# Optimization experiments

Measured on AMD Instinct MI355X. Metric: run time of the kernel, lower is better.

Reference implementation:

```python
import jax, jax.numpy as jnp
import numpy as np

B, C_IN, C_OUT, N, T, KT = 8, 32, 64, 512, 24, 3
EPS = 1e-5

def leaky(x):
    return jax.nn.leaky_relu(x, 0.01)

def layer_norm(x, g, b):
    # LayerNorm over last 3 dims [C_OUT, N, T]
    m = x.mean(axis=(1, 2, 3), keepdims=True)
    v = x.var(axis=(1, 2, 3), keepdims=True)
    return (x - m) * jax.lax.rsqrt(v + EPS) * g[None] + b[None]

def conv1d_dil2(x, w):
    # Conv1d(kernel=2, dilation=2, padding=1, no bias); x: (B,C,L), w: (O,C,2)
    return jax.lax.conv_general_dilated(x, w, window_strides=(1,), padding=[(1, 1)],
                                        rhs_dilation=(2,), dimension_numbers=('NCH', 'OIH', 'NCH'))

def setup_inputs():
    key = jax.random.key(0)
    ks = jax.random.split(key, 32)
    x = jax.random.normal(ks[0], (B, C_IN, N, T), jnp.float32)
    mask = jax.random.uniform(ks[1], (N, N)) < 0.02
    adj = jnp.where(mask, jax.random.uniform(ks[2], (N, N)), 0.0).astype(jnp.float32)
    s = 0.05
    p = {
        'conv1_w': jax.random.normal(ks[3], (C_OUT, C_IN)) * s,
        'conv1_b': jnp.zeros((C_OUT,)),
        'tc_w': jax.random.normal(ks[4], (C_OUT, C_IN, 1, KT)) * s,
        'tc_b': jnp.zeros((C_OUT,)),
        'ln_g': jnp.ones((C_OUT, N, T)),
        'ln_b': jnp.zeros((C_OUT, N, T)),
        's0_ws': jax.random.normal(ks[5], (T, T)) * s,
        's0_wn': jax.random.normal(ks[6], (T, T)) * s,
        's0_b': jnp.zeros((T,)),
        's1_ws': jax.random.normal(ks[7], (T, T)) * s,
        's1_wn': jax.random.normal(ks[8], (T, T)) * s,
        's1_b': jnp.zeros((T,)),
        't_w1': jax.random.normal(ks[9], (C_OUT,)) * s,
        't_w2': jax.random.normal(ks[10], (N,)) * s,
        't_wd1': jax.random.normal(ks[11], (T, T, 2)) * s,
        't_wd2': jax.random.normal(ks[12], (C_OUT, C_OUT, 2)) * s,
        't_W': jax.random.normal(ks[13], (N, C_OUT)) * s,
        't_b': jnp.zeros((T, T)),
        't_v': jax.random.normal(ks[14], (T, T)) * s,
        'bn_g': jnp.ones((T,)),
        'bn_b': jnp.zeros((T,)),
    }
    return {'x': x, 'adj': adj, **p}

def _forward(x, adj, conv1_w, conv1_b, tc_w, tc_b, ln_g, ln_b,
             s0_ws, s0_wn, s0_b, s1_ws, s1_wn, s1_b,
             t_w1, t_w2, t_wd1, t_wd2, t_W, t_b, t_v, bn_g, bn_b):
    # 1x1 conv residual branch
    x_input = jnp.einsum('bcnl,oc->bonl', x, conv1_w) + conv1_b[None, :, None, None]
    # temporal conv (1,Kt) padding (0,1)
    x1 = jax.lax.conv_general_dilated(x, tc_w, (1, 1), [(0, 0), (1, 1)],
                                      dimension_numbers=('NCHW', 'OIHW', 'NCHW'))
    x1 = x1 + tc_b[None, :, None, None]
    x1 = leaky(layer_norm(x1, ln_g, ln_b))
    Ls = jnp.stack([jnp.eye(N, dtype=x.dtype) * 4.0, adj])          # (2,N,N)
    h = jnp.einsum('bcnl,knq->bckql', x1, Ls)                        # (B,C_OUT,2,N,T)
    M = (adj != 0).astype(x.dtype)                                   # edges u->v
    deg = jnp.maximum(M.sum(axis=0), 1.0)                            # in-degree per dst
    def sage(h, ws, wn, bias):
        neigh = jnp.einsum('bckul,uv->bckvl', h, M) / deg[None, None, None, :, None]
        return (jnp.einsum('bcknl,ml->bcknm', h, ws)
                + jnp.einsum('bcknl,ml->bcknm', neigh, wn) + bias)
    h = sage(h, s0_ws, s0_wn, s0_b)
    h = sage(h, s1_ws, s1_wn, s1_b)
    x1 = h.reshape(B, 2 * C_OUT, N, T)
    filt, gate = x1[:, :C_OUT], x1[:, C_OUT:]
    x1 = jax.nn.sigmoid(gate) * leaky(filt)                          # (B,C_OUT,N,T)
    # TATT_1
    f1 = jnp.einsum('bcnl,c->bln', x1, t_w1)                         # (B,T,N)
    f1 = conv1d_dil2(f1, t_wd1)                                      # (B,T,N)
    f2 = jnp.einsum('bcnl,n->bcl', x1, t_w2)                         # (B,C_OUT,T)
    f2 = conv1d_dil2(f2, t_wd2)                                      # (B,C_OUT,T)
    logits = jax.nn.sigmoid(jnp.einsum('bln,nc,bcq->blq', f1, t_W, f2) + t_b)
    logits = jnp.einsum('lk,bkq->blq', t_v, logits)                  # (B,T,T)
    # BatchNorm1d(T) on permuted (B,T_q,T_l), training-mode batch stats
    z = logits.transpose(0, 2, 1)
    mu = z.mean(axis=(0, 2), keepdims=True)
    var = z.var(axis=(0, 2), keepdims=True)
    z = (z - mu) * jax.lax.rsqrt(var + EPS) * bn_g[None, :, None] + bn_b[None, :, None]
    logits = z.transpose(0, 2, 1)
    A = np.zeros((T, T), np.float32); A[:12, :12] = 1.0; A[12:, 12:] = 1.0
    Bmask = jnp.asarray(-1e13 * (1.0 - A), jnp.float32)
    coefs = jax.nn.softmax(logits + Bmask, axis=-1)                  # (B,T,T)
    T_coef = coefs.transpose(0, 2, 1)
    x1 = jnp.einsum('bcnl,blq->bcnq', x1, T_coef)
    out = layer_norm(leaky(x1) + x_input, ln_g, ln_b)
    return out, adj, T_coef

def reference(x, adj, conv1_w, conv1_b, tc_w, tc_b, ln_g, ln_b,
              s0_ws, s0_wn, s0_b, s1_ws, s1_wn, s1_b,
              t_w1, t_w2, t_wd1, t_wd2, t_W, t_b, t_v, bn_g, bn_b):
    return _forward(x, adj, conv1_w, conv1_b, tc_w, tc_b, ln_g, ln_b,
                    s0_ws, s0_wn, s0_b, s1_ws, s1_wn, s1_b,
                    t_w1, t_w2, t_wd1, t_wd2, t_W, t_b, t_v, bn_g, bn_b)
```

## Files before the change

kernel.cpp:

```cpp
#include <hip/hip_runtime.h>
#include <hip/hip_bf16.h>
#include <math.h>

#define B_    8
#define CIN   32
#define CO    64
#define NN    512
#define TT    24
#define NT    (NN*TT)
#define LNCNT (CO*NT)
#define EPSL  1e-5f
#define MAXNZ 64
#define HSS   28

typedef const float* fp;
static __device__ __forceinline__ float lk(float x){ return x > 0.f ? x : 0.01f*x; }
static __device__ __forceinline__ float sg(float x){
    if(x >= 0.f){ float e = expf(-x); return 1.f/(1.f+e); }
    float e = expf(x); return e/(1.f+e);
}
static __device__ __forceinline__ unsigned pk2(float a, float b){
    __hip_bfloat16 x = __float2bfloat16(a), y = __float2bfloat16(b);
    unsigned lo = *(unsigned short*)&x, hi = *(unsigned short*)&y;
    return lo | (hi<<16);
}
static __device__ __forceinline__ float lo2f(unsigned u){ return __uint_as_float(u<<16); }
static __device__ __forceinline__ float hi2f(unsigned u){ return __uint_as_float(u & 0xffff0000u); }

__global__ __launch_bounds__(256) void k_csc(fp adj, int* cnt, int* idx, float* val,
        float* o_adj){
    int e = blockIdx.x*blockDim.x + threadIdx.x;
    if(e >= NN*NN) return;
    float a = adj[e];
    o_adj[e] = a;
    if(a != 0.f){
        int u = e >> 9, q = e & 511;
        int slot = atomicAdd(&cnt[q], 1);
        if(slot < MAXNZ){ idx[q*MAXNZ+slot] = u; val[q*MAXNZ+slot] = a; }
    }
}

static __device__ __forceinline__ void ldw_split(fp w, int m, int kb, uint4* hi, uint4* lo){
    float vh[8], vl[8];
    #pragma unroll
    for(int j=0;j<8;++j){
        float v = (m < TT && (kb+j) < TT) ? w[m*TT + kb + j] : 0.f;
        __hip_bfloat16 hb = __float2bfloat16(v);
        float hf = __bfloat162float(hb);
        vh[j] = hf;
        vl[j] = v - hf;
    }
    *hi = make_uint4(pk2(vh[0],vh[1]),pk2(vh[2],vh[3]),pk2(vh[4],vh[5]),pk2(vh[6],vh[7]));
    *lo = make_uint4(pk2(vl[0],vl[1]),pk2(vl[2],vl[3]),pk2(vl[4],vl[5]),pk2(vl[6],vl[7]));
}

__global__ __launch_bounds__(256) void k_wprep(fp s0ws, fp s0wn, fp s1ws, fp s1wn, uint4* wf,
        fp w1, fp wt, uint4* wcf){
    int t = threadIdx.x;
    int lane = t & 63, g = t >> 6;
    {
        int M = g >> 1, H = g & 1;
        int m  = H*16 + (lane&15);
        int kb = (lane>>4)*8;
        for(int L=0; L<2; ++L){
            fp w = L ? (M ? s1wn : s1ws) : (M ? s0wn : s0ws);
            uint4 hi, lo;
            ldw_split(w, m, kb, &hi, &lo);
            wf[L*512 + g*128 +      lane] = hi;
            wf[L*512 + g*128 + 64 + lane] = lo;
        }
    }
    {
        int kb = (lane>>4)*8;
        for(int ot=0; ot<4; ++ot){
            int m = ot*16 + (lane&15);
            float vh[8], vl[8];
            #pragma unroll
            for(int j=0;j<8;++j){
                int c = kb+j;
                float v = (g==0) ? w1[m*CIN+c] : wt[(m*CIN+c)*3 + (g-1)];
                __hip_bfloat16 hb = __float2bfloat16(v);
                float hf = __bfloat162float(hb);
                vh[j]=hf; vl[j]=v-hf;
            }
            wcf[ot*512 + g*128 +      lane] = make_uint4(
                pk2(vh[0],vh[1]),pk2(vh[2],vh[3]),pk2(vh[4],vh[5]),pk2(vh[6],vh[7]));
            wcf[ot*512 + g*128 + 64 + lane] = make_uint4(
                pk2(vl[0],vl[1]),pk2(vl[2],vl[3]),pk2(vl[4],vl[5]),pk2(vl[6],vl[7]));
        }
    }
}

typedef __attribute__((ext_vector_type(8))) short bf16x8;
typedef __attribute__((ext_vector_type(4))) float f32x4;
typedef __attribute__((ext_vector_type(2))) float f32x2;

static __device__ __forceinline__ f32x4 MF(uint4 a, uint4 b, f32x4 c){
    union { uint4 u; bf16x8 v; } A, Bv; A.u = a; Bv.u = b;
    return __builtin_amdgcn_mfma_f32_16x16x32_bf16(A.v, Bv.v, c, 0, 0, 0);
}

#define XST 20
__global__ __launch_bounds__(256, 4) void k_conv(fp x, const uint4* wcf, fp b1, fp bt,
        float* xin, float* x1p, float* stats){
    __shared__ __attribute__((aligned(16))) unsigned xh[208*XST];
    __shared__ __attribute__((aligned(16))) unsigned xl[208*XST];
    __shared__ float red[256];
    int bid = blockIdx.x; int b = bid>>6; int n0 = (bid&63)*8;
    int tid = threadIdx.x; int lane = tid&63; int w = tid>>6;
    for(int i=tid;i<3072;i+=256){
        int cp = i/192; int r = i-cp*192; int node = r/24; int t = r-node*24;
        const float* xp = x + ((size_t)(b*CIN + 2*cp)*NN + n0+node)*TT + t;
        float a = xp[0], b2 = xp[NT];
        __hip_bfloat16 ab = __float2bfloat16(a), bb = __float2bfloat16(b2);
        float ah = __bfloat162float(ab), bh = __bfloat162float(bb);
        int row = node*26 + t + 1;
        xh[row*XST+cp] = pk2(ah, bh);
        xl[row*XST+cp] = pk2(a-ah, b2-bh);
    }
    {
        int node = tid>>5; int which = (tid>>4)&1; int j = tid&15;
        int row = node*26 + which*25;
        xh[row*XST+j]=0; xl[row*XST+j]=0;
    }
    const uint4* wb = wcf + w*512;
    uint4 h1 = wb[      lane], l1 = wb[ 64+lane];
    uint4 ht0= wb[128 + lane], lt0= wb[192+lane];
    uint4 ht1= wb[256 + lane], lt1= wb[320+lane];
    uint4 ht2= wb[384 + lane], lt2= wb[448+lane];
    int mrow = (lane>>4)*4;
    float bi0[4], bi1[4];
    #pragma unroll
    for(int r2=0;r2<4;++r2){
        int o = w*16 + mrow + r2;
        bi0[r2]=b1[o]; bi1[r2]=bt[o];
    }
    __syncthreads();
    float ls=0.f, lsq=0.f;
    int kb4 = (lane>>4)*4;
    for(int pt=0; pt<12; ++pt){
        int p = pt*16 + (lane&15);
        int node = p/24, t = p-node*24;
        int rc = (node*26 + t + 1)*XST;
        uint4 Bhm = *(const uint4*)&xh[rc - XST + kb4];
        uint4 Blm = *(const uint4*)&xl[rc - XST + kb4];
        uint4 Bhc = *(const uint4*)&xh[rc       + kb4];
        uint4 Blc = *(const uint4*)&xl[rc       + kb4];
        uint4 Bhp = *(const uint4*)&xh[rc + XST + kb4];
        uint4 Blp = *(const uint4*)&xl[rc + XST + kb4];
        f32x4 D0 = {bi0[0],bi0[1],bi0[2],bi0[3]};
        f32x4 D1 = {bi1[0],bi1[1],bi1[2],bi1[3]};
        D0 = MF(h1, Bhc, D0); D0 = MF(l1, Bhc, D0); D0 = MF(h1, Blc, D0);
        D1 = MF(ht0,Bhm, D1); D1 = MF(lt0,Bhm, D1); D1 = MF(ht0,Blm, D1);
        D1 = MF(ht1,Bhc, D1); D1 = MF(lt1,Bhc, D1); D1 = MF(ht1,Blc, D1);
        D1 = MF(ht2,Bhp, D1); D1 = MF(lt2,Bhp, D1); D1 = MF(ht2,Blp, D1);
        size_t gbase = ((size_t)(b*CO + w*16 + mrow)*NN + n0+node)*TT + t;
        #pragma unroll
        for(int r2=0;r2<4;++r2){
            xin[gbase + (size_t)r2*NT] = D0[r2];
            x1p[gbase + (size_t)r2*NT] = D1[r2];
            ls  += D1[r2];
            lsq += D1[r2]*D1[r2];
        }
    }
    red[tid]=ls; __syncthreads();
    for(int s=128;s>0;s>>=1){ if(tid<s) red[tid]+=red[tid+s]; __syncthreads(); }
    float tsum = red[0]; __syncthreads();
    red[tid]=lsq; __syncthreads();
    for(int s=128;s>0;s>>=1){ if(tid<s) red[tid]+=red[tid+s]; __syncthreads(); }
    if(tid==0){ atomicAdd(&stats[b], tsum); atomicAdd(&stats[8+b], red[0]); }
}

__global__ __launch_bounds__(512, 4) void k_hbuild(fp x1p, fp lng, fp lnb,
        const float* stats, const int* cnt, const int* idx, const float* val, unsigned* h){
    __shared__ float xs[NN*HSS];
    int blk = blockIdx.x; int b = blk >> 6; int c = blk & 63;
    int tid = threadIdx.x;
    float mm = stats[b] / (float)LNCNT;
    float vv = fmaxf(stats[8+b] / (float)LNCNT - mm*mm, 0.f);
    float m = mm, inv = rsqrtf(vv + EPSL);
    fp src  = x1p + (size_t)(b*CO + c)*NT;
    fp gsrc = lng + (size_t)c*NT;
    fp bsrc = lnb + (size_t)c*NT;
    for(int i4=tid;i4<NT/4;i4+=512){
        int i = i4*4;
        int n = i/TT, t = i-n*TT;
        float4 s  = *(const float4*)(src + i);
        float4 g  = *(const float4*)(gsrc + i);
        float4 bb = *(const float4*)(bsrc + i);
        *(float4*)&xs[n*HSS + t] = make_float4(
            lk((s.x-m)*inv*g.x+bb.x), lk((s.y-m)*inv*g.y+bb.y),
            lk((s.z-m)*inv*g.z+bb.z), lk((s.w-m)*inv*g.w+bb.w));
    }
    int n = tid;
    int c0 = cnt[n];
    int cq = c0 > MAXNZ ? MAXNZ : c0;
    int4 j0 = *(const int4*)&idx[n*MAXNZ+0];
    int4 j1 = *(const int4*)&idx[n*MAXNZ+4];
    int4 j2 = *(const int4*)&idx[n*MAXNZ+8];
    float4 v0 = *(const float4*)&val[n*MAXNZ+0];
    float4 v1 = *(const float4*)&val[n*MAXNZ+4];
    float4 v2 = *(const float4*)&val[n*MAXNZ+8];
    __syncthreads();
    float acc[TT];
    #pragma unroll
    for(int l=0;l<TT;++l) acc[l]=0.f;
#define HB(J,U,V) if((J)<cq){ const float4* rp=(const float4*)&xs[(U)*HSS]; \
    _Pragma("unroll") for(int k=0;k<6;++k){ float4 wv=rp[k]; \
        acc[4*k]+=(V)*wv.x; acc[4*k+1]+=(V)*wv.y; acc[4*k+2]+=(V)*wv.z; acc[4*k+3]+=(V)*wv.w; } }
    HB(0,j0.x,v0.x) HB(1,j0.y,v0.y) HB(2,j0.z,v0.z) HB(3,j0.w,v0.w)
    HB(4,j1.x,v1.x) HB(5,j1.y,v1.y) HB(6,j1.z,v1.z) HB(7,j1.w,v1.w)
    HB(8,j2.x,v2.x) HB(9,j2.y,v2.y) HB(10,j2.z,v2.z) HB(11,j2.w,v2.w)
    for(int j=12;j<cq;++j){
        int u = idx[n*MAXNZ+j]; float v = val[n*MAXNZ+j];
        const float4* rp = (const float4*)&xs[u*HSS];
        #pragma unroll
        for(int k=0;k<6;++k){ float4 wv=rp[k];
            acc[4*k]+=v*wv.x; acc[4*k+1]+=v*wv.y; acc[4*k+2]+=v*wv.z; acc[4*k+3]+=v*wv.w; }
    }
    float t1[TT];
    const float4* sp = (const float4*)&xs[n*HSS];
    #pragma unroll
    for(int k=0;k<6;++k){
        float4 v = sp[k];
        t1[4*k]=v.x; t1[4*k+1]=v.y; t1[4*k+2]=v.z; t1[4*k+3]=v.w;
    }
    unsigned* h0 = h + (size_t)((b*CO+c)*2)*(NT/2);
    unsigned* h1 = h0 + NT/2;
    #pragma unroll
    for(int k=0;k<3;++k){
        *(uint4*)(h0 + n*12 + 4*k) = make_uint4(
            pk2(4.f*t1[8*k],  4.f*t1[8*k+1]), pk2(4.f*t1[8*k+2],4.f*t1[8*k+3]),
            pk2(4.f*t1[8*k+4],4.f*t1[8*k+5]), pk2(4.f*t1[8*k+6],4.f*t1[8*k+7]));
        *(uint4*)(h1 + n*12 + 4*k) = make_uint4(
            pk2(acc[8*k],  acc[8*k+1]), pk2(acc[8*k+2],acc[8*k+3]),
            pk2(acc[8*k+4],acc[8*k+5]), pk2(acc[8*k+6],acc[8*k+7]));
    }
}

static __device__ __forceinline__ void acc8v(f32x2* t, uint4 q){
    t[0] += (f32x2){lo2f(q.x), hi2f(q.x)};
    t[1] += (f32x2){lo2f(q.y), hi2f(q.y)};
    t[2] += (f32x2){lo2f(q.z), hi2f(q.z)};
    t[3] += (f32x2){lo2f(q.w), hi2f(q.w)};
}

#define GBODY(u) { int ro=(u)*12; \
    uint4 q0=*(const uint4*)&hsb[ro]; \
    uint4 q1=*(const uint4*)&hsb[ro+4]; \
    uint4 q2=*(const uint4*)&hsb[ro+8]; \
    acc8v(t2v,q0); acc8v(t2v+4,q1); acc8v(t2v+8,q2); }
#define GSTEP(J,U) if((J)<cq) GBODY(U)

__global__ __launch_bounds__(512, 4) void k_sageF(unsigned* h, const uint4* wf,
        fp s0b, fp s1b, const int* cnt, const int* idx){
    __shared__ unsigned hsb[NN*12];
    int tid  = threadIdx.x;
    int lane = tid & 63;
    int wv   = tid >> 6;
    unsigned* base = h + (size_t)blockIdx.x*(NT/2);

    for(int i=tid;i<1536;i+=512) ((uint4*)hsb)[i] = ((const uint4*)base)[i];
    int n  = tid;
    int c0 = cnt[n];
    float di = 1.f / (float)(c0 < 1 ? 1 : c0);
    int cq = c0 > MAXNZ ? MAXNZ : c0;
    int4 i0 = *(const int4*)&idx[n*MAXNZ+0];
    int4 i1 = *(const int4*)&idx[n*MAXNZ+4];
    int4 i2 = *(const int4*)&idx[n*MAXNZ+8];
    __syncthreads();

    for(int layer=0; layer<2; ++layer){
        const uint4* wl = wf + layer*512;
        uint4 wsHiA = wl[      lane], wsLoA = wl[ 64+lane];
        uint4 wsHiB = wl[128 + lane], wsLoB = wl[192+lane];
        uint4 wnHiA = wl[256 + lane], wnLoA = wl[320+lane];
        uint4 wnHiB = wl[384 + lane], wnLoB = wl[448+lane];
        fp Bp = layer ? s1b : s0b;
        float biA[4], biB[4];
        #pragma unroll
        for(int r=0;r<4;++r){
            biA[r] = Bp[(lane>>4)*4 + r];
            int m2 = 16 + (lane>>4)*4 + r;
            biB[r] = (m2 < TT) ? Bp[m2] : 0.f;
        }

        f32x2 t2v[12];
        #pragma unroll
        for(int l=0;l<12;++l) t2v[l] = (f32x2){0.f,0.f};
        GSTEP(0,i0.x) GSTEP(1,i0.y) GSTEP(2,i0.z) GSTEP(3,i0.w)
        GSTEP(4,i1.x) GSTEP(5,i1.y) GSTEP(6,i1.z) GSTEP(7,i1.w)
        GSTEP(8,i2.x) GSTEP(9,i2.y) GSTEP(10,i2.z) GSTEP(11,i2.w)
        for(int j=12;j<cq;++j){ int u=idx[n*MAXNZ+j]; GBODY(u) }
        #pragma unroll
        for(int l=0;l<12;++l) t2v[l] *= di;

        uint4 b0[4];
        #pragma unroll
        for(int i=0;i<4;++i) b0[i]=make_uint4(0,0,0,0);
        if(lane < 48){
            #pragma unroll
            for(int i=0;i<4;++i){
                int nn_ = wv*64 + i*16 + (lane&15);
                b0[i] = *(const uint4*)&hsb[nn_*12 + ((lane>>4)<<2)];
            }
        }
        __syncthreads();

        *(uint4*)&hsb[n*12  ] = make_uint4(
            pk2(t2v[0].x,t2v[0].y), pk2(t2v[1].x,t2v[1].y),
            pk2(t2v[2].x,t2v[2].y), pk2(t2v[3].x,t2v[3].y));
        *(uint4*)&hsb[n*12+4] = make_uint4(
            pk2(t2v[4].x,t2v[4].y), pk2(t2v[5].x,t2v[5].y),
            pk2(t2v[6].x,t2v[6].y), pk2(t2v[7].x,t2v[7].y));
        *(uint4*)&hsb[n*12+8] = make_uint4(
            pk2(t2v[8].x,t2v[8].y), pk2(t2v[9].x,t2v[9].y),
            pk2(t2v[10].x,t2v[10].y), pk2(t2v[11].x,t2v[11].y));
        __syncthreads();

        uint4 b1[4];
        #pragma unroll
        for(int i=0;i<4;++i) b1[i]=make_uint4(0,0,0,0);
        if(lane < 48){
            #pragma unroll
            for(int i=0;i<4;++i){
                int nn_ = wv*64 + i*16 + (lane&15);
                b1[i] = *(const uint4*)&hsb[nn_*12 + ((lane>>4)<<2)];
            }
        }
        uint2 pa[4], pb[4];
        #pragma unroll
        for(int i=0;i<4;++i){
            f32x4 Da = {biA[0],biA[1],biA[2],biA[3]};
            f32x4 Db = {biB[0],biB[1],biB[2],biB[3]};
            Da = MF(wsHiA, b0[i], Da);
            Da = MF(wsLoA, b0[i], Da);
            Da = MF(wnHiA, b1[i], Da);
            Da = MF(wnLoA, b1[i], Da);
            Db = MF(wsHiB, b0[i], Db);
            Db = MF(wsLoB, b0[i], Db);
            Db = MF(wnHiB, b1[i], Db);
            Db = MF(wnLoB, b1[i], Db);
            pa[i] = make_uint2(pk2(Da[0],Da[1]), pk2(Da[2],Da[3]));
            pb[i] = make_uint2(pk2(Db[0],Db[1]), pk2(Db[2],Db[3]));
        }
        __syncthreads();
        #pragma unroll
        for(int i=0;i<4;++i){
            int nn_ = wv*64 + i*16 + (lane&15);
            int o = (lane>>4)*2;
            *(uint2*)&hsb[nn_*12 + o] = pa[i];
            if(lane < 32){
                *(uint2*)&hsb[nn_*12 + 8 + (lane>>4)*2] = pb[i];
            }
        }
        __syncthreads();
    }
    for(int i=tid;i<1536;i+=512) ((uint4*)base)[i] = ((const uint4*)hsb)[i];
}

#define F2S 25
__global__ __launch_bounds__(256) void k_f12(const unsigned* h, fp w1, fp w2,
        float* f1, float* f2){
    __shared__ float red[256*F2S];
    int tid = threadIdx.x;
    if(blockIdx.x < 512){
        if(tid < 192){
            int blk = blockIdx.x; int b = blk>>6; int n0 = (blk&63)*8;
            float acc = 0.f;
            const unsigned* fb = h + (size_t)b*CO*NT + n0*12;
            const unsigned* gb = fb + (size_t)CO*(NT/2);
            int e = tid;
            for(int c=0;c<CO;++c){
                float w = w1[c];
                unsigned f = fb[(size_t)c*(NT/2) + (e>>1)];
                unsigned g = gb[(size_t)c*(NT/2) + (e>>1)];
                float fv = (e&1) ? hi2f(f) : lo2f(f);
                float gv = (e&1) ? hi2f(g) : lo2f(g);
                acc += sg(gv)*lk(fv)*w;
            }
            int nl = e/TT, t = e%TT;
            f1[(b*TT+t)*NN + n0+nl] = acc;
        }
        return;
    }
    int blk = blockIdx.x - 512; int b = blk/CO; int c = blk%CO;
    float acc[TT];
    #pragma unroll
    for(int l=0;l<TT;++l) acc[l]=0.f;
    const unsigned* fb = h + (size_t)b*CO*NT + (size_t)c*(NT/2);
    const unsigned* gb = fb + (size_t)CO*(NT/2);
    for(int n=tid;n<NN;n+=256){
        float w = w2[n];
        #pragma unroll
        for(int k=0;k<3;++k){
            uint4 f = *(const uint4*)(fb + n*12 + 4*k);
            uint4 g = *(const uint4*)(gb + n*12 + 4*k);
            acc[8*k  ] += sg(lo2f(g.x))*lk(lo2f(f.x))*w;
            acc[8*k+1] += sg(hi2f(g.x))*lk(hi2f(f.x))*w;
            acc[8*k+2] += sg(lo2f(g.y))*lk(lo2f(f.y))*w;
            acc[8*k+3] += sg(hi2f(g.y))*lk(hi2f(f.y))*w;
            acc[8*k+4] += sg(lo2f(g.z))*lk(lo2f(f.z))*w;
            acc[8*k+5] += sg(hi2f(g.z))*lk(hi2f(f.z))*w;
            acc[8*k+6] += sg(lo2f(g.w))*lk(lo2f(f.w))*w;
            acc[8*k+7] += sg(hi2f(g.w))*lk(hi2f(f.w))*w;
        }
    }
    #pragma unroll
    for(int l=0;l<TT;++l) red[tid*F2S+l]=acc[l];
    __syncthreads();
    for(int s=128;s>0;s>>=1){
        if(tid<s){
            #pragma unroll
            for(int l=0;l<TT;++l) red[tid*F2S+l]+=red[(tid+s)*F2S+l];
        }
        __syncthreads();
    }
    if(tid<TT) f2[(b*CO+c)*TT+tid] = red[tid];
}

__global__ __launch_bounds__(256) void k_conv_f1(fp f1, fp wd1, float* f1c){
    __shared__ float fs[TT][130];
    __shared__ float w0[TT*TT], w1a[TT*TT];
    int bid = blockIdx.x; int b = bid>>2; int n0 = (bid&3)*128;
    int tid=threadIdx.x;
    for(int i=tid;i<TT*130;i+=256){
        int l=i/130, col=i%130; int n = n0+col-1;
        fs[l][col] = (n>=0 && n<NN) ? f1[(b*TT+l)*NN+n] : 0.f;
    }
    for(int i=tid;i<TT*TT;i+=256){ w0[i]=wd1[i*2]; w1a[i]=wd1[i*2+1]; }
    __syncthreads();
    for(int j=tid;j<TT*128;j+=256){
        int o=j>>7, nn=j&127;
        float acc=0.f;
        #pragma unroll
        for(int i=0;i<TT;++i) acc += fs[i][nn]*w0[o*TT+i] + fs[i][nn+2]*w1a[o*TT+i];
        f1c[(b*TT+o)*NN+n0+nn]=acc;
    }
}

__global__ __launch_bounds__(256) void k_conv_f2(fp f2, fp wd2, float* f2c){
    __shared__ float fs[CO][TT+2];
    __shared__ float w0[CO*CO], w1a[CO*CO];
    int b = blockIdx.x; int tid=threadIdx.x;
    for(int i=tid;i<CO*TT;i+=256){ int c=i/TT,l=i%TT; fs[c][l+1]=f2[(b*CO+c)*TT+l]; }
    for(int c=tid;c<CO;c+=256){ fs[c][0]=0.f; fs[c][TT+1]=0.f; }
    for(int i=tid;i<CO*CO;i+=256){ w0[i]=wd2[i*2]; w1a[i]=wd2[i*2+1]; }
    __syncthreads();
    for(int j=tid;j<CO*TT;j+=256){
        int o=j/TT, l=j%TT;
        float acc=0.f;
        for(int i=0;i<CO;++i) acc += fs[i][l]*w0[o*CO+i] + fs[i][l+2]*w1a[o*CO+i];
        f2c[(b*CO+o)*TT+l]=acc;
    }
}

__global__ __launch_bounds__(384) void k_g1(fp f1c, fp tW, float* g1){
    __shared__ float fs[6*NN];
    int blk=blockIdx.x; int b=blk>>2; int part=blk&3;
    int tid=threadIdx.x;
    for(int i=tid;i<6*NN;i+=384) fs[i]=f1c[b*TT*NN + part*6*NN + i];
    __syncthreads();
    int c = tid & 63; int r = tid >> 6;
    float acc=0.f;
    for(int n=0;n<NN;++n) acc += fs[r*NN + n]*tW[n*CO + c];
    g1[(b*TT + part*6 + r)*CO + c] = acc;
}

__global__ __launch_bounds__(256) void k_lgA(fp g1, fp f2c, fp tbias, float* sig){
    int j = blockIdx.x*256 + threadIdx.x;
    int b=j/(TT*TT); int r=j%(TT*TT); int l=r/TT; int q=r%TT;
    float acc = tbias[l*TT+q];
    fp gg = g1 + (b*TT+l)*CO;
    fp ff = f2c + b*CO*TT + q;
    for(int c=0;c<CO;++c) acc += gg[c]*ff[c*TT];
    sig[j] = sg(acc);
}
__global__ __launch_bounds__(256) void k_lgB(fp tv, const float* sig, float* lg2){
    int j = blockIdx.x*256 + threadIdx.x;
    int b=j/(TT*TT); int r=j%(TT*TT); int l=r/TT; int q=r%TT;
    float acc=0.f;
    for(int k=0;k<TT;++k) acc += tv[l*TT+k]*sig[(b*TT+k)*TT+q];
    lg2[j]=acc;
}
__global__ __launch_bounds__(256) void k_lgC(const float* lg2, fp bng, fp bnb,
        float* coefs, float* tco){
    __shared__ float muq[TT], scq[TT], shq[TT];
    int tid=threadIdx.x;
    if(tid<TT){
        int q=tid;
        float s=0.f;
        for(int b=0;b<B_;++b) for(int l=0;l<TT;++l) s += lg2[(b*TT+l)*TT+q];
        float mu = s/192.f;
        float v=0.f;
        for(int b=0;b<B_;++b) for(int l=0;l<TT;++l){ float d = lg2[(b*TT+l)*TT+q]-mu; v += d*d; }
        v = fmaxf(v/192.f, 0.f);
        muq[q]=mu; scq[q]=rsqrtf(v+EPSL)*bng[q]; shq[q]=bnb[q];
    }
    __syncthreads();
    if(tid<192){
        int b=tid/TT, l=tid%TT;
        int base = (l<12)?0:12;
        float z[12];
        float mx=-1e30f;
        #pragma unroll
        for(int r=0;r<12;++r){
            int q=base+r;
            float zv=(lg2[(b*TT+l)*TT+q]-muq[q])*scq[q]+shq[q];
            z[r]=zv; mx = fmaxf(mx,zv);
        }
        float s=0.f;
        #pragma unroll
        for(int r=0;r<12;++r){ z[r]=expf(z[r]-mx); s+=z[r]; }
        float is=1.f/s;
        for(int q=0;q<TT;++q){
            float cf = (q>=base && q<base+12) ? z[q-base]*is : 0.f;
            coefs[(b*TT+l)*TT+q]=cf;
            tco[(b*TT+q)*TT+l]=cf;
        }
    }
}

__global__ __launch_bounds__(256, 4) void k_apply(const unsigned* h, fp xin, fp coefs,
        float* y, float* stats){
    __shared__ float cf[TT*TT];
    __shared__ float red[256];
    int blk=blockIdx.x; int b=blk>>7; int c=(blk>>1)&63; int half=blk&1;
    int tid=threadIdx.x;
    for(int i=tid;i<TT*TT;i+=256) cf[i]=coefs[b*TT*TT+i];
    __syncthreads();
    int n = half*256 + tid;
    const unsigned* fb = h + (size_t)b*CO*NT + (size_t)c*(NT/2) + n*12;
    const unsigned* gb = fb + (size_t)CO*(NT/2);
    fp xrow = xin + (size_t)(b*CO+c)*NT + n*TT;
    float* yrow = y + (size_t)(b*CO+c)*NT + n*TT;
    float row[TT];
    #pragma unroll
    for(int k=0;k<3;++k){
        uint4 f = *(const uint4*)(fb + 4*k);
        uint4 g = *(const uint4*)(gb + 4*k);
        row[8*k  ] = sg(lo2f(g.x))*lk(lo2f(f.x));
        row[8*k+1] = sg(hi2f(g.x))*lk(hi2f(f.x));
        row[8*k+2] = sg(lo2f(g.y))*lk(lo2f(f.y));
        row[8*k+3] = sg(hi2f(g.y))*lk(hi2f(f.y));
        row[8*k+4] = sg(lo2f(g.z))*lk(lo2f(f.z));
        row[8*k+5] = sg(hi2f(g.z))*lk(hi2f(f.z));
        row[8*k+6] = sg(lo2f(g.w))*lk(lo2f(f.w));
        row[8*k+7] = sg(hi2f(g.w))*lk(hi2f(f.w));
    }
    float ls=0.f, lsq=0.f;
    #pragma unroll
    for(int k=0;k<6;++k){
        float4 u = *(const float4*)(xrow + 4*k);
        float a0=0.f, a1=0.f, a2=0.f, a3=0.f;
        #pragma unroll
        for(int l=0;l<TT;++l){
            float r = row[l];
            a0 += r*cf[(4*k  )*TT+l];
            a1 += r*cf[(4*k+1)*TT+l];
            a2 += r*cf[(4*k+2)*TT+l];
            a3 += r*cf[(4*k+3)*TT+l];
        }
        float y0 = lk(a0)+u.x, y1 = lk(a1)+u.y, y2 = lk(a2)+u.z, y3 = lk(a3)+u.w;
        *(float4*)(yrow + 4*k) = make_float4(y0,y1,y2,y3);
        ls  += y0+y1+y2+y3;
        lsq += y0*y0+y1*y1+y2*y2+y3*y3;
    }
    red[tid]=ls; __syncthreads();
    for(int s=128;s>0;s>>=1){ if(tid<s) red[tid]+=red[tid+s]; __syncthreads(); }
    float t0=red[0]; __syncthreads();
    red[tid]=lsq; __syncthreads();
    for(int s=128;s>0;s>>=1){ if(tid<s) red[tid]+=red[tid+s]; __syncthreads(); }
    if(tid==0){ atomicAdd(&stats[32+b], t0); atomicAdd(&stats[40+b], red[0]); }
}

__global__ void k_final(fp y, fp lng, fp lnb, const float* stats, float* out){
    float mb[8], sb[8];
    #pragma unroll
    for(int b=0;b<8;++b){
        float mm = stats[32+b] / (float)LNCNT;
        float vv = fmaxf(stats[40+b] / (float)LNCNT - mm*mm, 0.f);
        mb[b]=mm; sb[b]=rsqrtf(vv + EPSL);
    }
    int tot = B_*CO*NT;
    for(int i = blockIdx.x*blockDim.x + threadIdx.x; i<tot; i+=gridDim.x*blockDim.x){
        int b = i/LNCNT; int r = i%LNCNT;
        out[i] = (y[i]-mb[b])*sb[b]*lng[r]+lnb[r];
    }
}

extern "C" void kernel_launch(void* const* d_in, const int* in_sizes, int n_in,
                              void* d_out, int out_size, void* d_ws, size_t ws_size,
                              hipStream_t stream){
    fp x    = (fp)d_in[0];
    fp adj  = (fp)d_in[1];
    fp w1   = (fp)d_in[2];
    fp b1   = (fp)d_in[3];
    fp wt   = (fp)d_in[4];
    fp bt   = (fp)d_in[5];
    fp lng  = (fp)d_in[6];
    fp lnb  = (fp)d_in[7];
    fp s0ws = (fp)d_in[8];
    fp s0wn = (fp)d_in[9];
    fp s0b  = (fp)d_in[10];
    fp s1ws = (fp)d_in[11];
    fp s1wn = (fp)d_in[12];
    fp s1b  = (fp)d_in[13];
    fp tw1  = (fp)d_in[14];
    fp tw2  = (fp)d_in[15];
    fp twd1 = (fp)d_in[16];
    fp twd2 = (fp)d_in[17];
    fp tW   = (fp)d_in[18];
    fp tbias= (fp)d_in[19];
    fp tv   = (fp)d_in[20];
    fp bng  = (fp)d_in[21];
    fp bnb  = (fp)d_in[22];

    float* W = (float*)d_ws;
    int*   CNTp = (int*)(W+256);
    int*   IDXp = (int*)(W+1280);
    float* VALp = W+34048;
    float* F1   = W+66816;
    float* F1C  = W+165120;
    float* F2   = W+263424;
    float* F2C  = W+275712;
    float* G1   = W+288000;
    float* CF   = W+300288;
    float* XIN  = W+304896;
    float* X1   = W+6596352;
    float* SIG  = W+6596352;
    uint4* WFq  = (uint4*)(W+12887808);
    uint4* WCF  = (uint4*)(W+12891904);
    unsigned* HA = (unsigned*)(W+19179264);
    float* Y    = W+31762176;
    float* LG2  = SIG + 4608;

    float* oout   = (float*)d_out;
    float* o_adj  = oout + 6291456;
    float* o_tc   = oout + 6291456 + 262144;

    hipMemsetAsync(W, 0, 768*sizeof(float), stream);
    k_csc<<<1024,256,0,stream>>>(adj, CNTp, IDXp, VALp, o_adj);
    k_wprep<<<1,256,0,stream>>>(s0ws, s0wn, s1ws, s1wn, WFq, w1, wt, WCF);
    k_conv<<<512,256,0,stream>>>(x, WCF, b1, bt, XIN, X1, W);
    k_hbuild<<<512,512,0,stream>>>(X1, lng, lnb, W, CNTp, IDXp, VALp, HA);
    k_sageF<<<1024,512,0,stream>>>(HA, WFq, s0b, s1b, CNTp, IDXp);
    k_f12<<<1024,256,0,stream>>>(HA, tw1, tw2, F1, F2);
    k_conv_f1<<<32,256,0,stream>>>(F1, twd1, F1C);
    k_conv_f2<<<8,256,0,stream>>>(F2, twd2, F2C);
    k_g1<<<32,384,0,stream>>>(F1C, tW, G1);
    k_lgA<<<18,256,0,stream>>>(G1, F2C, tbias, SIG);
    k_lgB<<<18,256,0,stream>>>(tv, SIG, LG2);
    k_lgC<<<1,256,0,stream>>>(LG2, bng, bnb, CF, o_tc);
    k_apply<<<1024,256,0,stream>>>(HA, XIN, CF, Y, W);
    k_final<<<2048,256,0,stream>>>(Y, lng, lnb, W, oout);
}
```

Before: 357.1 us.

## Fuse logit kernels and split apply work across two threads per node

Merges k_lgB into the single-block BatchNorm/softmax kernel, so the 8x24x24 logits stay in shared memory and one launch is removed. k_apply now launches twice as many blocks: each node's 24 output time steps are split across two threads, and each thread reads the coefficient rows as float4 vectors from aligned shared memory. This raises parallelism and shortens each thread's serial work, at the cost of both threads redundantly unpacking the same gated h row and doubling the block-level reductions and atomics. The fused logit kernel now computes all 4608 logits with one block instead of 18 blocks.

```diff
diff --git a/kernel.cpp b/kernel.cpp
--- a/kernel.cpp
+++ b/kernel.cpp
@@ -476,17 +476,18 @@
     for(int c=0;c<CO;++c) acc += gg[c]*ff[c*TT];
     sig[j] = sg(acc);
 }
-__global__ __launch_bounds__(256) void k_lgB(fp tv, const float* sig, float* lg2){
-    int j = blockIdx.x*256 + threadIdx.x;
-    int b=j/(TT*TT); int r=j%(TT*TT); int l=r/TT; int q=r%TT;
-    float acc=0.f;
-    for(int k=0;k<TT;++k) acc += tv[l*TT+k]*sig[(b*TT+k)*TT+q];
-    lg2[j]=acc;
-}
-__global__ __launch_bounds__(256) void k_lgC(const float* lg2, fp bng, fp bnb,
-        float* coefs, float* tco){
+__global__ __launch_bounds__(256) void k_lgBC(fp tv, const float* sig,
+        fp bng, fp bnb, float* coefs, float* tco){
+    __shared__ float lg2[B_*TT*TT];
     __shared__ float muq[TT], scq[TT], shq[TT];
     int tid=threadIdx.x;
+    for(int j=tid;j<B_*TT*TT;j+=256){
+        int b=j/(TT*TT); int r=j%(TT*TT); int l=r/TT; int q=r%TT;
+        float acc=0.f;
+        for(int k=0;k<TT;++k) acc += tv[l*TT+k]*sig[(b*TT+k)*TT+q];
+        lg2[j]=acc;
+    }
+    __syncthreads();
     if(tid<TT){
         int q=tid;
         float s=0.f;
@@ -523,17 +524,18 @@
 
 __global__ __launch_bounds__(256, 4) void k_apply(const unsigned* h, fp xin, fp coefs,
         float* y, float* stats){
-    __shared__ float cf[TT*TT];
+    __shared__ __attribute__((aligned(16))) float cf[TT*TT];
     __shared__ float red[256];
-    int blk=blockIdx.x; int b=blk>>7; int c=(blk>>1)&63; int half=blk&1;
+    int blk=blockIdx.x; int b=blk>>8; int c=(blk>>2)&63; int quar=blk&3;
     int tid=threadIdx.x;
     for(int i=tid;i<TT*TT;i+=256) cf[i]=coefs[b*TT*TT+i];
     __syncthreads();
-    int n = half*256 + tid;
+    int nl = tid & 127, qh = tid >> 7;
+    int n = quar*128 + nl;
     const unsigned* fb = h + (size_t)b*CO*NT + (size_t)c*(NT/2) + n*12;
     const unsigned* gb = fb + (size_t)CO*(NT/2);
-    fp xrow = xin + (size_t)(b*CO+c)*NT + n*TT;
-    float* yrow = y + (size_t)(b*CO+c)*NT + n*TT;
+    fp xrow = xin + (size_t)(b*CO+c)*NT + n*TT + qh*12;
+    float* yrow = y + (size_t)(b*CO+c)*NT + n*TT + qh*12;
     float row[TT];
     #pragma unroll
     for(int k=0;k<3;++k){
@@ -550,18 +552,25 @@
     }
     float ls=0.f, lsq=0.f;
     #pragma unroll
-    for(int k=0;k<6;++k){
+    for(int k=0;k<3;++k){
         float4 u = *(const float4*)(xrow + 4*k);
-        float a0=0.f, a1=0.f, a2=0.f, a3=0.f;
-        #pragma unroll
-        for(int l=0;l<TT;++l){
-            float r = row[l];
-            a0 += r*cf[(4*k  )*TT+l];
-            a1 += r*cf[(4*k+1)*TT+l];
-            a2 += r*cf[(4*k+2)*TT+l];
-            a3 += r*cf[(4*k+3)*TT+l];
-        }
-        float y0 = lk(a0)+u.x, y1 = lk(a1)+u.y, y2 = lk(a2)+u.z, y3 = lk(a3)+u.w;
+        float a[4];
+        #pragma unroll
+        for(int j=0;j<4;++j){
+            int q = qh*12 + 4*k + j;
+            const float4* crow = (const float4*)&cf[q*TT];
+            float acc=0.f;
+            #pragma unroll
+            for(int kk=0;kk<6;++kk){
+                float4 cv = crow[kk];
+                acc += row[4*kk  ]*cv.x;
+                acc += row[4*kk+1]*cv.y;
+                acc += row[4*kk+2]*cv.z;
+                acc += row[4*kk+3]*cv.w;
+            }
+            a[j]=acc;
+        }
+        float y0 = lk(a[0])+u.x, y1 = lk(a[1])+u.y, y2 = lk(a[2])+u.z, y3 = lk(a[3])+u.w;
         *(float4*)(yrow + 4*k) = make_float4(y0,y1,y2,y3);
         ls  += y0+y1+y2+y3;
         lsq += y0*y0+y1*y1+y2*y2+y3*y3;
@@ -633,7 +642,6 @@
     uint4* WCF  = (uint4*)(W+12891904);
     unsigned* HA = (unsigned*)(W+19179264);
     float* Y    = W+31762176;
-    float* LG2  = SIG + 4608;
 
     float* oout   = (float*)d_out;
     float* o_adj  = oout + 6291456;
@@ -650,8 +658,7 @@
     k_conv_f2<<<8,256,0,stream>>>(F2, twd2, F2C);
     k_g1<<<32,384,0,stream>>>(F1C, tW, G1);
     k_lgA<<<18,256,0,stream>>>(G1, F2C, tbias, SIG);
-    k_lgB<<<18,256,0,stream>>>(tv, SIG, LG2);
-    k_lgC<<<1,256,0,stream>>>(LG2, bng, bnb, CF, o_tc);
-    k_apply<<<1024,256,0,stream>>>(HA, XIN, CF, Y, W);
+    k_lgBC<<<1,256,0,stream>>>(tv, SIG, bng, bnb, CF, o_tc);
+    k_apply<<<2048,256,0,stream>>>(HA, XIN, CF, Y, W);
     k_final<<<2048,256,0,stream>>>(Y, lng, lnb, W, oout);
 }
```

After: 384.5 us. 1.08x slower.
